# Kernel optimization log

Measured on AMD Instinct MI355X. Metric: run time of the kernel, lower is better.

## Reference

```python
import jax, jax.numpy as jnp
import numpy as np

HEADS = 4
C_HEAD = 32


def setup_inputs() -> dict:
    key = jax.random.key(0)
    k1, k2, k3 = jax.random.split(key, 3)
    c_in = 256
    c_hid = HEADS * C_HEAD  # 128
    x = jax.random.normal(k1, (4, c_in, 64, 64), dtype=jnp.float32)
    # 1x1 conv weights stored as [out, in]
    w_qkv = jax.random.normal(k2, (3 * c_hid, c_in), dtype=jnp.float32) * (c_in ** -0.5)
    w_out = jax.random.normal(k3, (c_in, c_hid), dtype=jnp.float32) * (c_hid ** -0.5)
    b_out = jnp.zeros((c_in,), dtype=jnp.float32)
    return {"x": x, "w_qkv": w_qkv, "w_out": w_out, "b_out": b_out}


def reference(x, w_qkv, w_out, b_out):
    b, c, h, w = x.shape
    scale = C_HEAD ** -0.5
    # 1x1 conv == channel matmul
    qkv = jnp.einsum('bchw,oc->bohw', x, w_qkv)  # [b, 3*c_hid, h, w]
    q, k, v = jnp.split(qkv, 3, axis=1)
    # b (heads c_head) x y -> b heads c_head (x y)
    def to_heads(t):
        return t.reshape(b, HEADS, C_HEAD, h * w)
    q, k, v = to_heads(q) * scale, to_heads(k), to_heads(v)
    sim = jnp.einsum('bhci,bhcj->bhij', q, k)  # [b, heads, N, N]
    sim = sim - jax.lax.stop_gradient(jnp.max(sim, axis=-1, keepdims=True))
    attn = jax.nn.softmax(sim, axis=-1)
    out = jnp.einsum('bhij,bhcj->bhic', attn, v)  # [b, heads, N, c_head]
    # b h (x y) c -> b (h c) x y
    out = out.transpose(0, 1, 3, 2).reshape(b, HEADS * C_HEAD, h, w)
    out = jnp.einsum('bchw,oc->bohw', out, w_out) + b_out[None, :, None, None]
    return out
```

## Files before the change

### kernel.cpp

```cpp
#include <hip/hip_runtime.h>
#include <hip/hip_bf16.h>
#include <cstdint>
#include <cstddef>

#define NB 4
#define CIN 256
#define CHID 128
#define HEADS 4
#define CHEAD 32
#define NPOS 4096
#define BH 16
#define NTOT 16384
#define QKV_O 384
#define QSCALE_LOG2E 0.2550348229f

typedef float f32x4 __attribute__((ext_vector_type(4)));
typedef short s16x8 __attribute__((ext_vector_type(8)));

static __device__ __forceinline__ unsigned short f2bf(float f) {
    union { float f; unsigned u; } v; v.f = f;
    unsigned r = v.u + 0x7FFFu + ((v.u >> 16) & 1u);
    return (unsigned short)(r >> 16);
}

static __device__ __forceinline__ unsigned int pk2bf(float a, float b) {
    union { __hip_bfloat162 h; unsigned int u; } c;
    c.h = __float22bfloat162_rn(float2{a, b});
    return c.u;
}

static __device__ __forceinline__ void async_cp16(const void* g, void* l) {
    __builtin_amdgcn_global_load_lds((const __attribute__((address_space(1))) unsigned int*)g,
                                     (__attribute__((address_space(3))) unsigned int*)l, 16, 0, 0);
}

__global__ void k_convert_w(const float* __restrict__ wqkv, const float* __restrict__ wout,
                            unsigned short* __restrict__ wqkv_bf, unsigned short* __restrict__ wout_bf) {
    int i = blockIdx.x * 256 + threadIdx.x;
    if (i < QKV_O * CIN) wqkv_bf[i] = f2bf(wqkv[i]);
    if (i < CIN * CHID)  wout_bf[i]  = f2bf(wout[i]);
}

__global__ __launch_bounds__(256) void k_transpose_x(const float* __restrict__ x,
                                                     unsigned short* __restrict__ xT) {
    __shared__ float tile[32][33];
    const int ntiles = NPOS / 32;
    const int ctiles = CIN / 32;
    int b   = blockIdx.x / (ntiles * ctiles);
    int rem = blockIdx.x % (ntiles * ctiles);
    int ct = rem / ntiles;
    int nt = rem % ntiles;
    int c0 = ct * 32, n0 = nt * 32;
    int tc = threadIdx.x / 32;
    int tn = threadIdx.x % 32;
    const float* xb = x + (size_t)b * CIN * NPOS;
#pragma unroll
    for (int it = 0; it < 4; ++it) {
        int c = tc + it * 8;
        tile[c][tn] = xb[(size_t)(c0 + c) * NPOS + n0 + tn];
    }
    __syncthreads();
    unsigned short* xTb = xT + (size_t)b * NPOS * CIN;
#pragma unroll
    for (int it = 0; it < 4; ++it) {
        int n = tc + it * 8;
        xTb[(size_t)(n0 + n) * CIN + c0 + tn] = f2bf(tile[tn][n]);
    }
}

__global__ __launch_bounds__(256, 4) void k_qkv(const unsigned short* __restrict__ wq,
                                                const unsigned short* __restrict__ xT,
                                                unsigned short* __restrict__ Q,
                                                unsigned short* __restrict__ K,
                                                unsigned short* __restrict__ V) {
    __shared__ __align__(16) unsigned char smem[2 * 12288];
    int mt = blockIdx.x % 3;
    int nt = blockIdx.x / 3;
    int wid = threadIdx.x >> 6, lane = threadIdx.x & 63;
    int quad = lane >> 4, low4 = lane & 15;
    int o0 = mt * 128, n0 = nt * 64;
    int lb = lane * 16;

    const unsigned short* srcA0 = wq + (size_t)(o0 + wid * 32 + low4) * CIN + quad * 8;
    const unsigned short* srcA1 = srcA0 + 16 * CIN;
    const unsigned short* srcB  = xT + (size_t)(n0 + wid * 16 + low4) * CIN + quad * 8;
    int dA0 = wid * 2048, dA1 = dA0 + 1024, dB = 8192 + wid * 1024;

    async_cp16(srcA0, smem + dA0 + lb);
    async_cp16(srcA1, smem + dA1 + lb);
    async_cp16(srcB,  smem + dB  + lb);
    __syncthreads();

    f32x4 acc[2][4] = {};
    for (int c = 0; c < 8; ++c) {
        if (c < 7) {
            unsigned char* nxt = smem + ((c + 1) & 1) * 12288;
            async_cp16(srcA0 + (c + 1) * 32, nxt + dA0 + lb);
            async_cp16(srcA1 + (c + 1) * 32, nxt + dA1 + lb);
            async_cp16(srcB  + (c + 1) * 32, nxt + dB  + lb);
        }
        const unsigned char* cur = smem + (c & 1) * 12288;
        s16x8 a0 = *(const s16x8*)(cur + wid * 2048 + lb);
        s16x8 a1 = *(const s16x8*)(cur + wid * 2048 + 1024 + lb);
#pragma unroll
        for (int j = 0; j < 4; ++j) {
            s16x8 bj = *(const s16x8*)(cur + 8192 + j * 1024 + lb);
            acc[0][j] = __builtin_amdgcn_mfma_f32_16x16x32_bf16(a0, bj, acc[0][j], 0, 0, 0);
            acc[1][j] = __builtin_amdgcn_mfma_f32_16x16x32_bf16(a1, bj, acc[1][j], 0, 0, 0);
        }
        __syncthreads();
    }

#pragma unroll
    for (int i = 0; i < 2; ++i) {
        int ob = o0 + wid * 32 + i * 16 + quad * 4;
#pragma unroll
        for (int j = 0; j < 4; ++j) {
            int nG = n0 + j * 16 + low4;
            int b = nG >> 12, n = nG & 4095;
            f32x4 v = acc[i][j];
            if (ob < 128) {
                int head = ob >> 5, ch = ob & 31;
                unsigned long long d =
                    (unsigned long long)pk2bf(v[0] * QSCALE_LOG2E, v[1] * QSCALE_LOG2E) |
                    ((unsigned long long)pk2bf(v[2] * QSCALE_LOG2E, v[3] * QSCALE_LOG2E) << 32);
                *(unsigned long long*)(Q + ((size_t)(b * 4 + head) * NPOS + n) * 32 + ch) = d;
            } else if (ob < 256) {
                int o2 = ob - 128; int head = o2 >> 5, ch = o2 & 31;
                unsigned long long d =
                    (unsigned long long)pk2bf(v[0], v[1]) |
                    ((unsigned long long)pk2bf(v[2], v[3]) << 32);
                *(unsigned long long*)(K + ((size_t)(b * 4 + head) * NPOS + n) * 32 + ch) = d;
            } else {
#pragma unroll
                for (int r = 0; r < 4; ++r) {
                    int o2 = ob + r - 256; int head = o2 >> 5, ch = o2 & 31;
                    V[((size_t)((b * 4 + head) * 32 + ch)) * NPOS + n] = f2bf(v[r]);
                }
            }
        }
    }
}

__global__ __launch_bounds__(256, 4) void k_attn(const unsigned short* __restrict__ Q,
                                                 const unsigned short* __restrict__ K,
                                                 const unsigned short* __restrict__ V,
                                                 unsigned short* __restrict__ attnO) {
    __shared__ __align__(16) unsigned char smem[2 * 8192 + 4 * 2048];
    unsigned char* kv = smem;
    unsigned char* pT = smem + 16384;

    int bh  = blockIdx.x >> 6;
    int qt  = blockIdx.x & 63;
    int wid = threadIdx.x >> 6, lane = threadIdx.x & 63;
    int quad = lane >> 4, low4 = lane & 15;
    int q0w = qt * 64 + wid * 16;

    const unsigned short* Qp  = Q + (size_t)bh * NPOS * 32;
    const unsigned short* Kbh = K + (size_t)bh * NPOS * 32;
    const unsigned short* Vbh = V + (size_t)bh * 32 * NPOS;

    const unsigned short* gs0;
    size_t sstep; int ldsA;
    if (wid < 2) {
        gs0 = Kbh + (size_t)(wid * 32 + low4) * 32 + quad * 8;
        sstep = (size_t)64 * 32;
        ldsA = wid * 2048;
    } else {
        int c = wid - 2;
        gs0 = Vbh + (size_t)(c * 16 + low4) * NPOS + quad * 8;
        sstep = 64;
        ldsA = 4096 + c * 2048;
    }
    const unsigned short* gs1 = gs0 + ((wid < 2) ? 512 : 32);

    s16x8 bq = *(const s16x8*)(Qp + (size_t)(q0w + low4) * 32 + quad * 8);

    f32x4 oc0 = {}, oc1 = {};
    float lsum = 0.0f;

    unsigned char* pwave = pT + wid * 2048;
    unsigned char* pw = pwave + (quad >> 1) * 256 + low4 * 16 + (quad & 1) * 8;
    const int lby = lane * 16;

    async_cp16(gs0, kv + ldsA);
    async_cp16(gs1, kv + ldsA + 1024);
    __syncthreads();

    for (int it = 0; it < NPOS / 64; ++it) {
        if (it + 1 < NPOS / 64) {
            unsigned char* dst = kv + ((it + 1) & 1) * 8192 + ldsA;
            async_cp16(gs0 + (size_t)(it + 1) * sstep, dst);
            async_cp16(gs1 + (size_t)(it + 1) * sstep, dst + 1024);
        }
        const unsigned char* kb = kv + (it & 1) * 8192;
        s16x8 ak0  = *(const s16x8*)(kb + lby);
        s16x8 ak1  = *(const s16x8*)(kb + 1024 + lby);
        s16x8 ak2  = *(const s16x8*)(kb + 2048 + lby);
        s16x8 ak3  = *(const s16x8*)(kb + 3072 + lby);
        s16x8 av00 = *(const s16x8*)(kb + 4096 + lby);
        s16x8 av01 = *(const s16x8*)(kb + 5120 + lby);
        s16x8 av10 = *(const s16x8*)(kb + 6144 + lby);
        s16x8 av11 = *(const s16x8*)(kb + 7168 + lby);

        f32x4 s[4];
        s[0] = __builtin_amdgcn_mfma_f32_16x16x32_bf16(ak0, bq, f32x4{}, 0, 0, 0);
        s[1] = __builtin_amdgcn_mfma_f32_16x16x32_bf16(ak1, bq, f32x4{}, 0, 0, 0);
        s[2] = __builtin_amdgcn_mfma_f32_16x16x32_bf16(ak2, bq, f32x4{}, 0, 0, 0);
        s[3] = __builtin_amdgcn_mfma_f32_16x16x32_bf16(ak3, bq, f32x4{}, 0, 0, 0);

#pragma unroll
        for (int t = 0; t < 4; ++t) {
            float p0 = __builtin_amdgcn_exp2f(s[t][0]);
            float p1 = __builtin_amdgcn_exp2f(s[t][1]);
            float p2 = __builtin_amdgcn_exp2f(s[t][2]);
            float p3 = __builtin_amdgcn_exp2f(s[t][3]);
            lsum += (p0 + p1) + (p2 + p3);
            unsigned long long d = (unsigned long long)pk2bf(p0, p1)
                                 | ((unsigned long long)pk2bf(p2, p3) << 32);
            *(unsigned long long*)(pw + (t >> 1) * 1024 + (t & 1) * 512) = d;
        }
        s16x8 bp0 = *(const s16x8*)(pwave + lby);
        s16x8 bp1 = *(const s16x8*)(pwave + 1024 + lby);

        oc0 = __builtin_amdgcn_mfma_f32_16x16x32_bf16(av00, bp0, oc0, 0, 0, 0);
        oc1 = __builtin_amdgcn_mfma_f32_16x16x32_bf16(av10, bp0, oc1, 0, 0, 0);
        oc0 = __builtin_amdgcn_mfma_f32_16x16x32_bf16(av01, bp1, oc0, 0, 0, 0);
        oc1 = __builtin_amdgcn_mfma_f32_16x16x32_bf16(av11, bp1, oc1, 0, 0, 0);

        __syncthreads();
    }

    lsum += __shfl_xor(lsum, 16);
    lsum += __shfl_xor(lsum, 32);
    float inv = 1.0f / lsum;

    int b = bh >> 2, head = bh & 3;
    int n = q0w + low4;
#pragma unroll
    for (int c = 0; c < 2; ++c) {
        f32x4 o = c == 0 ? oc0 : oc1;
        int ch = head * 32 + c * 16 + quad * 4;
        unsigned long long d =
            (unsigned long long)pk2bf(o[0] * inv, o[1] * inv) |
            ((unsigned long long)pk2bf(o[2] * inv, o[3] * inv) << 32);
        *(unsigned long long*)(attnO + ((size_t)(b * NPOS + n)) * CHID + ch) = d;
    }
}

__global__ __launch_bounds__(256, 4) void k_out(const unsigned short* __restrict__ wo,
                                                const unsigned short* __restrict__ attnO,
                                                const float* __restrict__ bias,
                                                float* __restrict__ out) {
    __shared__ __align__(16) unsigned char smem[2 * 12288];
    int mt = blockIdx.x & 1;
    int nt = blockIdx.x >> 1;
    int wid = threadIdx.x >> 6, lane = threadIdx.x & 63;
    int quad = lane >> 4, low4 = lane & 15;
    int o0 = mt * 128, n0 = nt * 64;
    int lb = lane * 16;

    const unsigned short* srcA0 = wo + (size_t)(o0 + wid * 32 + low4) * CHID + quad * 8;
    const unsigned short* srcA1 = srcA0 + 16 * CHID;
    const unsigned short* srcB  = attnO + (size_t)(n0 + wid * 16 + low4) * CHID + quad * 8;
    int dA0 = wid * 2048, dA1 = dA0 + 1024, dB = 8192 + wid * 1024;

    async_cp16(srcA0, smem + dA0 + lb);
    async_cp16(srcA1, smem + dA1 + lb);
    async_cp16(srcB,  smem + dB  + lb);
    __syncthreads();

    f32x4 acc[2][4] = {};
    for (int c = 0; c < 4; ++c) {
        if (c < 3) {
            unsigned char* nxt = smem + ((c + 1) & 1) * 12288;
            async_cp16(srcA0 + (c + 1) * 32, nxt + dA0 + lb);
            async_cp16(srcA1 + (c + 1) * 32, nxt + dA1 + lb);
            async_cp16(srcB  + (c + 1) * 32, nxt + dB  + lb);
        }
        const unsigned char* cur = smem + (c & 1) * 12288;
        s16x8 a0 = *(const s16x8*)(cur + wid * 2048 + lb);
        s16x8 a1 = *(const s16x8*)(cur + wid * 2048 + 1024 + lb);
#pragma unroll
        for (int j = 0; j < 4; ++j) {
            s16x8 bj = *(const s16x8*)(cur + 8192 + j * 1024 + lb);
            acc[0][j] = __builtin_amdgcn_mfma_f32_16x16x32_bf16(a0, bj, acc[0][j], 0, 0, 0);
            acc[1][j] = __builtin_amdgcn_mfma_f32_16x16x32_bf16(a1, bj, acc[1][j], 0, 0, 0);
        }
        __syncthreads();
    }

#pragma unroll
    for (int i = 0; i < 2; ++i) {
        int ob = o0 + wid * 32 + i * 16 + quad * 4;
#pragma unroll
        for (int j = 0; j < 4; ++j) {
            int nG = n0 + j * 16 + low4;
            int b = nG >> 12, n = nG & 4095;
#pragma unroll
            for (int r = 0; r < 4; ++r) {
                int o = ob + r;
                out[((size_t)(b * CIN + o)) * NPOS + n] = acc[i][j][r] + bias[o];
            }
        }
    }
}

extern "C" void kernel_launch(void* const* d_in, const int* in_sizes, int n_in,
                              void* d_out, int out_size, void* d_ws, size_t ws_size,
                              hipStream_t stream) {
    const float* x    = (const float*)d_in[0];
    const float* wqkv = (const float*)d_in[1];
    const float* wout = (const float*)d_in[2];
    const float* bout = (const float*)d_in[3];
    float* out = (float*)d_out;

    unsigned short* Q       = (unsigned short*)d_ws;
    unsigned short* K       = Q + (size_t)BH * NPOS * 32;
    unsigned short* V       = K + (size_t)BH * NPOS * 32;
    unsigned short* attnO   = V + (size_t)BH * 32 * NPOS;
    unsigned short* xT      = attnO + (size_t)NTOT * CHID;
    unsigned short* wqkv_bf = xT + (size_t)NTOT * CIN;
    unsigned short* wout_bf = wqkv_bf + QKV_O * CIN;

    k_convert_w<<<(QKV_O * CIN + 255) / 256, 256, 0, stream>>>(wqkv, wout, wqkv_bf, wout_bf);
    k_transpose_x<<<NB * (CIN / 32) * (NPOS / 32), 256, 0, stream>>>(x, xT);
    k_qkv<<<3 * (NTOT / 64), 256, 0, stream>>>(wqkv_bf, xT, Q, K, V);
    k_attn<<<BH * (NPOS / 64), 256, 0, stream>>>(Q, K, V, attnO);
    k_out<<<2 * (NTOT / 64), 256, 0, stream>>>(wout_bf, attnO, bout, out);
}
```

Measured before the change: 164.1 us.

## Rewrite attention kernel with 32x32 MFMA, in-register P transpose and split-K waves

The attention kernel moves from 16x16x32 to 32x32x16 bf16 MFMA tiles, with each wave handling 64 queries. The softmax probabilities stay in registers and are rearranged with permlane32_swap instead of a round trip through LDS. The key range is split between wave pairs, and their partial outputs and row sums are merged through shared memory at the end. This is meant to cut LDS traffic and raise MFMA efficiency, at the cost of fewer blocks, lower occupancy (launch bounds 2) and an extra reduction step.

After: 153.6 us. 6.4% less time.

```diff
diff --git a/kernel.cpp b/kernel.cpp
--- a/kernel.cpp
+++ b/kernel.cpp
@@ -15,6 +15,7 @@
 #define QSCALE_LOG2E 0.2550348229f
 
 typedef float f32x4 __attribute__((ext_vector_type(4)));
+typedef float f32x16 __attribute__((ext_vector_type(16)));
 typedef short s16x8 __attribute__((ext_vector_type(8)));
 
 static __device__ __forceinline__ unsigned short f2bf(float f) {
@@ -29,10 +30,33 @@
     return c.u;
 }
 
+static __device__ __forceinline__ void plswap(unsigned& a, unsigned& b) {
+#if __has_builtin(__builtin_amdgcn_permlane32_swap)
+    auto r = __builtin_amdgcn_permlane32_swap((int)a, (int)b, false, false);
+    a = (unsigned)r[0];
+    b = (unsigned)r[1];
+#else
+    int hh = (threadIdx.x >> 5) & 1;
+    unsigned ta = (unsigned)__shfl_xor((int)a, 32);
+    unsigned tb = (unsigned)__shfl_xor((int)b, 32);
+    unsigned na = hh ? tb : a;
+    unsigned nb = hh ? b : ta;
+    a = na; b = nb;
+#endif
+}
+
+static __device__ __forceinline__ s16x8 mk8(unsigned a, unsigned b, unsigned c, unsigned d) {
+    union { unsigned u[4]; s16x8 v; } x;
+    x.u[0] = a; x.u[1] = b; x.u[2] = c; x.u[3] = d;
+    return x.v;
+}
+
 static __device__ __forceinline__ void async_cp16(const void* g, void* l) {
     __builtin_amdgcn_global_load_lds((const __attribute__((address_space(1))) unsigned int*)g,
                                      (__attribute__((address_space(3))) unsigned int*)l, 16, 0, 0);
 }
+
+#define MFMA32(a, b, c) __builtin_amdgcn_mfma_f32_32x32x16_bf16(a, b, c, 0, 0, 0)
 
 __global__ void k_convert_w(const float* __restrict__ wqkv, const float* __restrict__ wout,
                             unsigned short* __restrict__ wqkv_bf, unsigned short* __restrict__ wout_bf) {
@@ -142,109 +166,134 @@
     }
 }
 
-__global__ __launch_bounds__(256, 4) void k_attn(const unsigned short* __restrict__ Q,
+__global__ __launch_bounds__(256, 2) void k_attn(const unsigned short* __restrict__ Q,
                                                  const unsigned short* __restrict__ K,
                                                  const unsigned short* __restrict__ V,
                                                  unsigned short* __restrict__ attnO) {
-    __shared__ __align__(16) unsigned char smem[2 * 8192 + 4 * 2048];
-    unsigned char* kv = smem;
-    unsigned char* pT = smem + 16384;
-
-    int bh  = blockIdx.x >> 6;
-    int qt  = blockIdx.x & 63;
+    __shared__ __align__(16) unsigned char smem[2 * 16384];
+    int bh = blockIdx.x & 15;
+    int qt = blockIdx.x >> 4;
     int wid = threadIdx.x >> 6, lane = threadIdx.x & 63;
-    int quad = lane >> 4, low4 = lane & 15;
-    int q0w = qt * 64 + wid * 16;
+    int q5 = lane & 31, h = lane >> 5;
+    int qg = wid & 1, kh = wid >> 1;
+    int q0 = qt * 128 + qg * 64;
+    int khk = kh * 2048;
 
     const unsigned short* Qp  = Q + (size_t)bh * NPOS * 32;
     const unsigned short* Kbh = K + (size_t)bh * NPOS * 32;
     const unsigned short* Vbh = V + (size_t)bh * 32 * NPOS;
 
-    const unsigned short* gs0;
-    size_t sstep; int ldsA;
-    if (wid < 2) {
-        gs0 = Kbh + (size_t)(wid * 32 + low4) * 32 + quad * 8;
-        sstep = (size_t)64 * 32;
-        ldsA = wid * 2048;
-    } else {
-        int c = wid - 2;
-        gs0 = Vbh + (size_t)(c * 16 + low4) * NPOS + quad * 8;
-        sstep = 64;
-        ldsA = 4096 + c * 2048;
-    }
-    const unsigned short* gs1 = gs0 + ((wid < 2) ? 512 : 32);
-
-    s16x8 bq = *(const s16x8*)(Qp + (size_t)(q0w + low4) * 32 + quad * 8);
-
-    f32x4 oc0 = {}, oc1 = {};
-    float lsum = 0.0f;
-
-    unsigned char* pwave = pT + wid * 2048;
-    unsigned char* pw = pwave + (quad >> 1) * 256 + low4 * 16 + (quad & 1) * 8;
+    s16x8 bq00 = *(const s16x8*)(Qp + (size_t)(q0 + q5) * 32 + h * 8);
+    s16x8 bq01 = *(const s16x8*)(Qp + (size_t)(q0 + q5) * 32 + 16 + h * 8);
+    s16x8 bq10 = *(const s16x8*)(Qp + (size_t)(q0 + 32 + q5) * 32 + h * 8);
+    s16x8 bq11 = *(const s16x8*)(Qp + (size_t)(q0 + 32 + q5) * 32 + 16 + h * 8);
+
+    const unsigned short* sK = Kbh + (size_t)q5 * 32 + h * 8;
+    const unsigned short* sV = Vbh + (size_t)q5 * NPOS + h * 8;
+    unsigned char* wbase0 = smem + kh * 8192;
+    unsigned char* wbase1 = smem + 16384 + kh * 8192;
+
+    auto stage = [&](int bufi, int k0) {
+        unsigned char* wb = bufi ? wbase1 : wbase0;
+        if (qg == 0) {
+            const unsigned short* p = sK + (size_t)k0 * 32;
+            async_cp16(p,        wb);
+            async_cp16(p + 16,   wb + 1024);
+            async_cp16(p + 1024, wb + 2048);
+            async_cp16(p + 1040, wb + 3072);
+        } else {
+            const unsigned short* p = sV + k0;
+            async_cp16(p,      wb + 4096);
+            async_cp16(p + 16, wb + 5120);
+            async_cp16(p + 32, wb + 6144);
+            async_cp16(p + 48, wb + 7168);
+        }
+    };
+
+    f32x16 oT0 = {}, oT1 = {};
+    float lsum0 = 0.0f, lsum1 = 0.0f;
     const int lby = lane * 16;
 
-    async_cp16(gs0, kv + ldsA);
-    async_cp16(gs1, kv + ldsA + 1024);
-    __syncthreads();
-
-    for (int it = 0; it < NPOS / 64; ++it) {
-        if (it + 1 < NPOS / 64) {
-            unsigned char* dst = kv + ((it + 1) & 1) * 8192 + ldsA;
-            async_cp16(gs0 + (size_t)(it + 1) * sstep, dst);
-            async_cp16(gs1 + (size_t)(it + 1) * sstep, dst + 1024);
-        }
-        const unsigned char* kb = kv + (it & 1) * 8192;
-        s16x8 ak0  = *(const s16x8*)(kb + lby);
-        s16x8 ak1  = *(const s16x8*)(kb + 1024 + lby);
-        s16x8 ak2  = *(const s16x8*)(kb + 2048 + lby);
-        s16x8 ak3  = *(const s16x8*)(kb + 3072 + lby);
-        s16x8 av00 = *(const s16x8*)(kb + 4096 + lby);
-        s16x8 av01 = *(const s16x8*)(kb + 5120 + lby);
-        s16x8 av10 = *(const s16x8*)(kb + 6144 + lby);
-        s16x8 av11 = *(const s16x8*)(kb + 7168 + lby);
-
-        f32x4 s[4];
-        s[0] = __builtin_amdgcn_mfma_f32_16x16x32_bf16(ak0, bq, f32x4{}, 0, 0, 0);
-        s[1] = __builtin_amdgcn_mfma_f32_16x16x32_bf16(ak1, bq, f32x4{}, 0, 0, 0);
-        s[2] = __builtin_amdgcn_mfma_f32_16x16x32_bf16(ak2, bq, f32x4{}, 0, 0, 0);
-        s[3] = __builtin_amdgcn_mfma_f32_16x16x32_bf16(ak3, bq, f32x4{}, 0, 0, 0);
-
-#pragma unroll
-        for (int t = 0; t < 4; ++t) {
-            float p0 = __builtin_amdgcn_exp2f(s[t][0]);
-            float p1 = __builtin_amdgcn_exp2f(s[t][1]);
-            float p2 = __builtin_amdgcn_exp2f(s[t][2]);
-            float p3 = __builtin_amdgcn_exp2f(s[t][3]);
-            lsum += (p0 + p1) + (p2 + p3);
-            unsigned long long d = (unsigned long long)pk2bf(p0, p1)
-                                 | ((unsigned long long)pk2bf(p2, p3) << 32);
-            *(unsigned long long*)(pw + (t >> 1) * 1024 + (t & 1) * 512) = d;
-        }
-        s16x8 bp0 = *(const s16x8*)(pwave + lby);
-        s16x8 bp1 = *(const s16x8*)(pwave + 1024 + lby);
-
-        oc0 = __builtin_amdgcn_mfma_f32_16x16x32_bf16(av00, bp0, oc0, 0, 0, 0);
-        oc1 = __builtin_amdgcn_mfma_f32_16x16x32_bf16(av10, bp0, oc1, 0, 0, 0);
-        oc0 = __builtin_amdgcn_mfma_f32_16x16x32_bf16(av01, bp1, oc0, 0, 0, 0);
-        oc1 = __builtin_amdgcn_mfma_f32_16x16x32_bf16(av11, bp1, oc1, 0, 0, 0);
-
+    stage(0, khk);
+    __syncthreads();
+
+#pragma unroll 1
+    for (int it = 0; it < 32; ++it) {
+        if (it + 1 < 32) stage((it + 1) & 1, khk + (it + 1) * 64);
+        const unsigned char* kb = smem + (it & 1) * 16384 + kh * 8192;
+#pragma unroll
+        for (int t = 0; t < 2; ++t) {
+            s16x8 ak0 = *(const s16x8*)(kb + t * 2048 + lby);
+            s16x8 ak1 = *(const s16x8*)(kb + t * 2048 + 1024 + lby);
+            f32x16 s0 = {}, s1 = {};
+            s0 = MFMA32(ak0, bq00, s0); s0 = MFMA32(ak1, bq01, s0);
+            s1 = MFMA32(ak0, bq10, s1); s1 = MFMA32(ak1, bq11, s1);
+            unsigned p0[8], p1[8];
+#pragma unroll
+            for (int i = 0; i < 8; ++i) {
+                float a0 = __builtin_amdgcn_exp2f(s0[2 * i]);
+                float a1 = __builtin_amdgcn_exp2f(s0[2 * i + 1]);
+                float b0 = __builtin_amdgcn_exp2f(s1[2 * i]);
+                float b1 = __builtin_amdgcn_exp2f(s1[2 * i + 1]);
+                lsum0 += a0 + a1;
+                lsum1 += b0 + b1;
+                p0[i] = pk2bf(a0, a1);
+                p1[i] = pk2bf(b0, b1);
+            }
+            plswap(p0[0], p0[2]); plswap(p0[1], p0[3]);
+            plswap(p0[4], p0[6]); plswap(p0[5], p0[7]);
+            plswap(p1[0], p1[2]); plswap(p1[1], p1[3]);
+            plswap(p1[4], p1[6]); plswap(p1[5], p1[7]);
+            s16x8 bp0lo = mk8(p0[0], p0[1], p0[2], p0[3]);
+            s16x8 bp0hi = mk8(p0[4], p0[5], p0[6], p0[7]);
+            s16x8 bp1lo = mk8(p1[0], p1[1], p1[2], p1[3]);
+            s16x8 bp1hi = mk8(p1[4], p1[5], p1[6], p1[7]);
+
+            s16x8 av0 = *(const s16x8*)(kb + 4096 + (2 * t) * 1024 + lby);
+            s16x8 av1 = *(const s16x8*)(kb + 4096 + (2 * t + 1) * 1024 + lby);
+            oT0 = MFMA32(av0, bp0lo, oT0); oT0 = MFMA32(av1, bp0hi, oT0);
+            oT1 = MFMA32(av0, bp1lo, oT1); oT1 = MFMA32(av1, bp1hi, oT1);
+        }
         __syncthreads();
     }
 
-    lsum += __shfl_xor(lsum, 16);
-    lsum += __shfl_xor(lsum, 32);
-    float inv = 1.0f / lsum;
-
-    int b = bh >> 2, head = bh & 3;
-    int n = q0w + low4;
-#pragma unroll
-    for (int c = 0; c < 2; ++c) {
-        f32x4 o = c == 0 ? oc0 : oc1;
-        int ch = head * 32 + c * 16 + quad * 4;
-        unsigned long long d =
-            (unsigned long long)pk2bf(o[0] * inv, o[1] * inv) |
-            ((unsigned long long)pk2bf(o[2] * inv, o[3] * inv) << 32);
-        *(unsigned long long*)(attnO + ((size_t)(b * NPOS + n)) * CHID + ch) = d;
+    lsum0 += __shfl_xor(lsum0, 32);
+    lsum1 += __shfl_xor(lsum1, 32);
+
+    float* area = (float*)smem + qg * 2176;
+    if (kh) {
+#pragma unroll
+        for (int j = 0; j < 4; ++j) {
+            *(f32x4*)(area + j * 256 + lane * 4) =
+                f32x4{oT0[4 * j], oT0[4 * j + 1], oT0[4 * j + 2], oT0[4 * j + 3]};
+            *(f32x4*)(area + 1024 + j * 256 + lane * 4) =
+                f32x4{oT1[4 * j], oT1[4 * j + 1], oT1[4 * j + 2], oT1[4 * j + 3]};
+        }
+        area[2048 + lane * 2]     = lsum0;
+        area[2048 + lane * 2 + 1] = lsum1;
+    }
+    __syncthreads();
+    if (!kh) {
+        lsum0 += area[2048 + lane * 2];
+        lsum1 += area[2048 + lane * 2 + 1];
+        float inv0 = 1.0f / lsum0, inv1 = 1.0f / lsum1;
+        int b = bh >> 2, head = bh & 3;
+        int n0 = q0 + q5, n1 = q0 + 32 + q5;
+        unsigned short* base0 = attnO + ((size_t)(b * NPOS + n0)) * CHID + head * 32 + 4 * h;
+        unsigned short* base1 = attnO + ((size_t)(b * NPOS + n1)) * CHID + head * 32 + 4 * h;
+#pragma unroll
+        for (int j = 0; j < 4; ++j) {
+            f32x4 r0 = *(const f32x4*)(area + j * 256 + lane * 4);
+            f32x4 r1 = *(const f32x4*)(area + 1024 + j * 256 + lane * 4);
+            unsigned long long d0 =
+                (unsigned long long)pk2bf((oT0[4 * j] + r0[0]) * inv0, (oT0[4 * j + 1] + r0[1]) * inv0) |
+                ((unsigned long long)pk2bf((oT0[4 * j + 2] + r0[2]) * inv0, (oT0[4 * j + 3] + r0[3]) * inv0) << 32);
+            *(unsigned long long*)(base0 + 8 * j) = d0;
+            unsigned long long d1 =
+                (unsigned long long)pk2bf((oT1[4 * j] + r1[0]) * inv1, (oT1[4 * j + 1] + r1[1]) * inv1) |
+                ((unsigned long long)pk2bf((oT1[4 * j + 2] + r1[2]) * inv1, (oT1[4 * j + 3] + r1[3]) * inv1) << 32);
+            *(unsigned long long*)(base1 + 8 * j) = d1;
+        }
     }
 }
 
@@ -326,6 +375,6 @@
     k_convert_w<<<(QKV_O * CIN + 255) / 256, 256, 0, stream>>>(wqkv, wout, wqkv_bf, wout_bf);
     k_transpose_x<<<NB * (CIN / 32) * (NPOS / 32), 256, 0, stream>>>(x, xT);
     k_qkv<<<3 * (NTOT / 64), 256, 0, stream>>>(wqkv_bf, xT, Q, K, V);
-    k_attn<<<BH * (NPOS / 64), 256, 0, stream>>>(Q, K, V, attnO);
+    k_attn<<<(NPOS / 128) * BH, 256, 0, stream>>>(Q, K, V, attnO);
     k_out<<<2 * (NTOT / 64), 256, 0, stream>>>(wout_bf, attnO, bout, out);
 }
```
